# Kernel tuning notes

Measured on AMD Instinct MI355X. Metric: run time of the kernel, lower is better.

## Reference

```python
import jax, jax.numpy as jnp
import numpy as np

H, I, E, TOP_K = 2048, 1408, 16, 6
IS = 2816  # shared-expert intermediate = moe_intermediate_size * n_shared_experts
NORM_TOPK_PROB = False


def _silu_and_mul(gate_up):
    # gate_up: [..., 2*I] -> silu(gate) * up, [..., I]
    d = gate_up.shape[-1] // 2
    g, u = gate_up[..., :d], gate_up[..., d:]
    return jax.nn.silu(g) * u


def setup_inputs() -> dict:
    key = jax.random.key(0)
    ks = jax.random.split(key, 6)
    s = 0.02
    return {
        "x": jax.random.normal(ks[0], (1, 2048, H), jnp.float32),
        "gate_w": jax.random.normal(ks[1], (E, H), jnp.float32) * s,
        "w1": jax.random.normal(ks[2], (E, 2 * I, H), jnp.float32) * s,
        "w2": jax.random.normal(ks[3], (E, H, I), jnp.float32) * s,
        "shared_w1": jax.random.normal(ks[4], (2 * IS, H), jnp.float32) * s,
        "shared_w2": jax.random.normal(ks[5], (H, IS), jnp.float32) * s,
    }


def reference(x, gate_w, w1, w2, shared_w1, shared_w2):
    B, S, Hd = x.shape
    xf = x.reshape(-1, Hd)  # [T, H]
    T = xf.shape[0]

    # shared experts (dense MLP over all tokens)
    shared_out = _silu_and_mul(xf @ shared_w1.T) @ shared_w2.T  # [T, H]

    # router: softmax in fp32, then top-k
    logits = xf @ gate_w.T  # [T, E]
    probs = jax.nn.softmax(logits.astype(jnp.float32), axis=-1)
    routing_weights, selected = jax.lax.top_k(probs, TOP_K)  # [T, k]
    if NORM_TOPK_PROB:
        routing_weights = routing_weights / routing_weights.sum(-1, keepdims=True)

    # scatter top-k weights into dense [T, E] combine matrix (fused_moe equivalent)
    combine = jnp.zeros((T, E), jnp.float32).at[
        jnp.arange(T)[:, None], selected
    ].add(routing_weights).astype(x.dtype)

    # expert MLPs, combined with routing weights
    gate_up = jnp.einsum('th,eoh->teo', xf, w1)  # [T, E, 2I]
    act = _silu_and_mul(gate_up)                 # [T, E, I]
    moe_out = jnp.einsum('te,tei,ehi->th', combine, act, w2)  # [T, H]

    return (moe_out + shared_out).reshape(B, S, Hd)
```

## Files before the change

### kernel.cpp

```cpp
#include <hip/hip_runtime.h>
#include <hip/hip_bf16.h>
#include <cstdint>
#include <cstddef>


typedef __bf16 bf16;
typedef __bf16 bf16x8 __attribute__((ext_vector_type(8)));
typedef float  f32x4  __attribute__((ext_vector_type(4)));

constexpr int Hdim  = 2048;
constexpr int Idim  = 1408;
constexpr int NE    = 16;
constexpr int TOPK  = 6;
constexpr int ISdim = 2816;
constexpr int Ttok  = 2048;
constexpr int MAX_SLOTS = 14336;

__device__ __forceinline__ void gll16(const bf16* g, bf16* l) {
  __builtin_amdgcn_global_load_lds((__attribute__((address_space(1))) void*)(g),
                                   (__attribute__((address_space(3))) void*)(l),
                                   16, 0, 0);
}


__global__ void init_kernel(int* cnt, int* fill, int* tok_of_slot, float* wt_of_slot) {
  int i = blockIdx.x * 256 + threadIdx.x;
  if (i < NE) { cnt[i] = 0; fill[i] = 0; }
  if (i < MAX_SLOTS) { tok_of_slot[i] = -1; wt_of_slot[i] = 0.f; }
}

__global__ void cvt_x_kernel(const float* __restrict__ x, bf16* __restrict__ xb) {
  int i = (blockIdx.x * 256 + threadIdx.x) * 8;
  f32x4 f0 = *(const f32x4*)(x + i);
  f32x4 f1 = *(const f32x4*)(x + i + 4);
  bf16x8 v;
#pragma unroll
  for (int j = 0; j < 4; j++) { v[j] = (bf16)f0[j]; v[j + 4] = (bf16)f1[j]; }
  *(bf16x8*)(xb + i) = v;
}

__global__ void router_kernel(const float* __restrict__ x, const float* __restrict__ gw,
                              int* __restrict__ sel_e, float* __restrict__ sel_w,
                              int* __restrict__ cnt) {
  int t = blockIdx.x;
  int lane = threadIdx.x;
  const float* xr = x + (size_t)t * Hdim;
  float acc[NE];
#pragma unroll
  for (int e = 0; e < NE; e++) acc[e] = 0.f;
  for (int h = lane; h < Hdim; h += 64) {
    float xv = xr[h];
#pragma unroll
    for (int e = 0; e < NE; e++) acc[e] += xv * gw[e * Hdim + h];
  }
#pragma unroll
  for (int e = 0; e < NE; e++) {
#pragma unroll
    for (int off = 32; off > 0; off >>= 1) acc[e] += __shfl_xor(acc[e], off, 64);
  }
  if (lane == 0) {
    float m = acc[0];
#pragma unroll
    for (int e = 1; e < NE; e++) m = fmaxf(m, acc[e]);
    float p[NE]; float s = 0.f;
#pragma unroll
    for (int e = 0; e < NE; e++) { p[e] = __expf(acc[e] - m); s += p[e]; }
    float inv = 1.f / s;
    bool used[NE];
#pragma unroll
    for (int e = 0; e < NE; e++) used[e] = false;
    for (int k = 0; k < TOPK; k++) {
      int best = 0; float bv = -1.f;
      for (int e = 0; e < NE; e++) if (!used[e] && p[e] > bv) { bv = p[e]; best = e; }
      used[best] = true;
      sel_e[t * TOPK + k] = best;
      sel_w[t * TOPK + k] = bv * inv;
      atomicAdd(&cnt[best], 1);
    }
  }
}

__global__ void scan_kernel(const int* __restrict__ cnt, int* __restrict__ pbase,
                            int* __restrict__ mtiles) {
  if (threadIdx.x == 0 && blockIdx.x == 0) {
    int pb = 0;
    for (int e = 0; e < NE; e++) {
      pbase[e] = pb;
      int mt = (cnt[e] + 127) >> 7;
      mtiles[e] = mt;
      pb += mt * 128;
    }
  }
}

__global__ void assign_kernel(const int* __restrict__ sel_e, const float* __restrict__ sel_w,
                              const int* __restrict__ pbase, int* __restrict__ fill,
                              int* __restrict__ tok_of_slot, float* __restrict__ wt_of_slot) {
  int i = blockIdx.x * 256 + threadIdx.x;
  if (i >= Ttok * TOPK) return;
  int t = i / TOPK;
  int e = sel_e[i];
  int pos = atomicAdd(&fill[e], 1);
  int slot = pbase[e] + pos;
  tok_of_slot[slot] = t;
  wt_of_slot[slot] = sel_w[i];
}


template <bool GROUPED>
__global__ __launch_bounds__(256, 2)
void gateup_kernel(const bf16* __restrict__ Abase, const float* __restrict__ W,
                   bf16* __restrict__ Cact,
                   const int* __restrict__ tok_of_slot, const float* __restrict__ wt_of_slot,
                   const int* __restrict__ pbase, const int* __restrict__ mtiles,
                   int K, int Isz) {
  const int e = GROUPED ? blockIdx.z : 0;
  const int mt = blockIdx.y;
  if (GROUPED) { if (mt >= mtiles[e]) return; }
  const int row0 = (GROUPED ? pbase[e] : 0) + mt * 128;
  const int col0 = blockIdx.x * 64;
  const int tid = threadIdx.x;
  const int lane = tid & 63;
  const int wv = tid >> 6;
  const int wm = wv >> 1, wn = wv & 1;
  const int m16 = lane & 15, quad = lane >> 4;

  __shared__ __align__(16) bf16 ldsA[128 * 32];
  __shared__ __align__(16) bf16 ldsG[64 * 32];
  __shared__ __align__(16) bf16 ldsU[64 * 32];

  const int srow = tid >> 2;
  const int scol = (tid & 3) * 8;

  const bf16* aptr[2];
#pragma unroll
  for (int q = 0; q < 2; q++) {
    int r = row0 + q * 64 + srow;
    int tok = GROUPED ? tok_of_slot[r] : r;
    if (GROUPED && tok < 0) tok = 0;
    aptr[q] = Abase + (size_t)tok * K + scol;
  }
  const float* Wb = W + (size_t)e * 2 * Isz * K;
  const float* Grow = Wb + (size_t)(col0 + srow) * K + scol;
  const float* Urow = Wb + (size_t)(Isz + col0 + srow) * K + scol;

  f32x4 accg[4][2], accu[4][2];
#pragma unroll
  for (int i = 0; i < 4; i++)
#pragma unroll
    for (int j = 0; j < 2; j++)
#pragma unroll
      for (int r = 0; r < 4; r++) { accg[i][j][r] = 0.f; accu[i][j][r] = 0.f; }

  f32x4 gb0 = *(const f32x4*)(Grow);
  f32x4 gb1 = *(const f32x4*)(Grow + 4);
  f32x4 ub0 = *(const f32x4*)(Urow);
  f32x4 ub1 = *(const f32x4*)(Urow + 4);

  for (int k0 = 0; k0 < K; k0 += 32) {
    bf16x8 gv, uv;
#pragma unroll
    for (int j = 0; j < 4; j++) {
      gv[j] = (bf16)gb0[j]; gv[j + 4] = (bf16)gb1[j];
      uv[j] = (bf16)ub0[j]; uv[j + 4] = (bf16)ub1[j];
    }
    *(bf16x8*)(&ldsG[tid * 8]) = gv;
    *(bf16x8*)(&ldsU[tid * 8]) = uv;
#pragma unroll
    for (int q = 0; q < 2; q++) gll16(aptr[q] + k0, &ldsA[q * 2048 + tid * 8]);
    if (k0 + 32 < K) {
      gb0 = *(const f32x4*)(Grow + k0 + 32);
      gb1 = *(const f32x4*)(Grow + k0 + 36);
      ub0 = *(const f32x4*)(Urow + k0 + 32);
      ub1 = *(const f32x4*)(Urow + k0 + 36);
    }
    __syncthreads();
    bf16x8 af[4], gf[2], uf[2];
#pragma unroll
    for (int i = 0; i < 4; i++)
      af[i] = *(const bf16x8*)(&ldsA[(wm * 64 + i * 16 + m16) * 32 + quad * 8]);
#pragma unroll
    for (int j = 0; j < 2; j++) {
      gf[j] = *(const bf16x8*)(&ldsG[(wn * 32 + j * 16 + m16) * 32 + quad * 8]);
      uf[j] = *(const bf16x8*)(&ldsU[(wn * 32 + j * 16 + m16) * 32 + quad * 8]);
    }
#pragma unroll
    for (int i = 0; i < 4; i++)
#pragma unroll
      for (int j = 0; j < 2; j++) {
        accg[i][j] = __builtin_amdgcn_mfma_f32_16x16x32_bf16(af[i], gf[j], accg[i][j], 0, 0, 0);
        accu[i][j] = __builtin_amdgcn_mfma_f32_16x16x32_bf16(af[i], uf[j], accu[i][j], 0, 0, 0);
      }
    __syncthreads();
  }

#pragma unroll
  for (int i = 0; i < 4; i++) {
#pragma unroll
    for (int r = 0; r < 4; r++) {
      int grow = row0 + wm * 64 + i * 16 + quad * 4 + r;
      float scale = 1.f;
      if (GROUPED) scale = wt_of_slot[grow];
#pragma unroll
      for (int j = 0; j < 2; j++) {
        float g = accg[i][j][r];
        float u = accu[i][j][r];
        float a = g * u * scale / (1.f + __expf(-g));
        Cact[(size_t)grow * Isz + (col0 + wn * 32 + j * 16 + m16)] = (bf16)a;
      }
    }
  }
}


template <bool GROUPED>
__global__ __launch_bounds__(256, 2)
void down_kernel(const bf16* __restrict__ A, const float* __restrict__ W,
                 float* __restrict__ out, const int* __restrict__ tok_of_slot,
                 const int* __restrict__ pbase, const int* __restrict__ mtiles, int K) {
  const int e = GROUPED ? blockIdx.z : 0;
  const int mt = blockIdx.y;
  if (GROUPED) { if (mt >= mtiles[e]) return; }
  const int row0 = (GROUPED ? pbase[e] : 0) + mt * 128;
  const int col0 = blockIdx.x * 128;
  const int tid = threadIdx.x;
  const int lane = tid & 63;
  const int wv = tid >> 6;
  const int wm = wv >> 1, wn = wv & 1;
  const int m16 = lane & 15, quad = lane >> 4;

  __shared__ __align__(16) bf16 ldsA[128 * 32];
  __shared__ __align__(16) bf16 ldsB[128 * 32];

  const int srow = tid >> 2;
  const int scol = (tid & 3) * 8;

  const bf16* aptr[2];
#pragma unroll
  for (int q = 0; q < 2; q++)
    aptr[q] = A + (size_t)(row0 + q * 64 + srow) * K + scol;
  const float* Wb = W + (size_t)e * Hdim * K;
  const float* Brow[2];
#pragma unroll
  for (int q = 0; q < 2; q++)
    Brow[q] = Wb + (size_t)(col0 + q * 64 + srow) * K + scol;

  f32x4 acc[4][4];
#pragma unroll
  for (int i = 0; i < 4; i++)
#pragma unroll
    for (int j = 0; j < 4; j++)
#pragma unroll
      for (int r = 0; r < 4; r++) acc[i][j][r] = 0.f;

  f32x4 bb[2][2];
#pragma unroll
  for (int q = 0; q < 2; q++) {
    bb[q][0] = *(const f32x4*)(Brow[q]);
    bb[q][1] = *(const f32x4*)(Brow[q] + 4);
  }

  for (int k0 = 0; k0 < K; k0 += 32) {
#pragma unroll
    for (int q = 0; q < 2; q++) {
      bf16x8 bv;
#pragma unroll
      for (int j = 0; j < 4; j++) { bv[j] = (bf16)bb[q][0][j]; bv[j + 4] = (bf16)bb[q][1][j]; }
      *(bf16x8*)(&ldsB[q * 2048 + tid * 8]) = bv;
      gll16(aptr[q] + k0, &ldsA[q * 2048 + tid * 8]);
    }
    if (k0 + 32 < K) {
#pragma unroll
      for (int q = 0; q < 2; q++) {
        bb[q][0] = *(const f32x4*)(Brow[q] + k0 + 32);
        bb[q][1] = *(const f32x4*)(Brow[q] + k0 + 36);
      }
    }
    __syncthreads();
    bf16x8 af[4], bfr[4];
#pragma unroll
    for (int i = 0; i < 4; i++)
      af[i] = *(const bf16x8*)(&ldsA[(wm * 64 + i * 16 + m16) * 32 + quad * 8]);
#pragma unroll
    for (int j = 0; j < 4; j++)
      bfr[j] = *(const bf16x8*)(&ldsB[(wn * 64 + j * 16 + m16) * 32 + quad * 8]);
#pragma unroll
    for (int i = 0; i < 4; i++)
#pragma unroll
      for (int j = 0; j < 4; j++)
        acc[i][j] = __builtin_amdgcn_mfma_f32_16x16x32_bf16(af[i], bfr[j], acc[i][j], 0, 0, 0);
    __syncthreads();
  }

#pragma unroll
  for (int i = 0; i < 4; i++) {
#pragma unroll
    for (int r = 0; r < 4; r++) {
      int grow = row0 + wm * 64 + i * 16 + quad * 4 + r;
      int tok;
      if (GROUPED) {
        tok = tok_of_slot[grow];
        if (tok < 0) continue;
      } else {
        tok = grow;
      }
      float* orow = out + (size_t)tok * Hdim;
#pragma unroll
      for (int j = 0; j < 4; j++) {
        int col = col0 + wn * 64 + j * 16 + m16;
        if (GROUPED) atomicAdd(orow + col, acc[i][j][r]);
        else orow[col] = acc[i][j][r];
      }
    }
  }
}


extern "C" void kernel_launch(void* const* d_in, const int* in_sizes, int n_in,
                              void* d_out, int out_size, void* d_ws, size_t ws_size,
                              hipStream_t stream) {
  (void)in_sizes; (void)n_in; (void)out_size; (void)ws_size;
  const float* x   = (const float*)d_in[0];
  const float* gw  = (const float*)d_in[1];
  const float* w1  = (const float*)d_in[2];
  const float* w2  = (const float*)d_in[3];
  const float* sw1 = (const float*)d_in[4];
  const float* sw2 = (const float*)d_in[5];
  float* out = (float*)d_out;

  char* ws = (char*)d_ws;
  size_t off = 0;
  auto alloc = [&](size_t bytes) -> void* {
    void* p = ws + off;
    off += (bytes + 255) & ~(size_t)255;
    return p;
  };
  int*   cnt   = (int*)alloc(NE * 4);
  int*   fill  = (int*)alloc(NE * 4);
  int*   pbase = (int*)alloc(NE * 4);
  int*   mtl   = (int*)alloc(NE * 4);
  int*   sel_e = (int*)alloc((size_t)Ttok * TOPK * 4);
  float* sel_w = (float*)alloc((size_t)Ttok * TOPK * 4);
  int*   tok   = (int*)alloc((size_t)MAX_SLOTS * 4);
  float* wt    = (float*)alloc((size_t)MAX_SLOTS * 4);
  bf16*  xb    = (bf16*)alloc((size_t)Ttok * Hdim * 2);
  bf16*  actx  = (bf16*)alloc((size_t)MAX_SLOTS * Idim * 2);
  bf16*  acts  = (bf16*)alloc((size_t)Ttok * ISdim * 2);

  init_kernel<<<(MAX_SLOTS + 255) / 256, 256, 0, stream>>>(cnt, fill, tok, wt);
  cvt_x_kernel<<<(Ttok * Hdim / 8 + 255) / 256, 256, 0, stream>>>(x, xb);
  router_kernel<<<Ttok, 64, 0, stream>>>(x, gw, sel_e, sel_w, cnt);
  scan_kernel<<<1, 64, 0, stream>>>(cnt, pbase, mtl);
  assign_kernel<<<(Ttok * TOPK + 255) / 256, 256, 0, stream>>>(sel_e, sel_w, pbase, fill, tok, wt);

  gateup_kernel<true><<<dim3(Idim / 64, 16, NE), 256, 0, stream>>>(
      xb, w1, actx, tok, wt, pbase, mtl, Hdim, Idim);
  gateup_kernel<false><<<dim3(ISdim / 64, Ttok / 128, 1), 256, 0, stream>>>(
      xb, sw1, acts, nullptr, nullptr, nullptr, nullptr, Hdim, ISdim);
  down_kernel<false><<<dim3(Hdim / 128, Ttok / 128, 1), 256, 0, stream>>>(
      acts, sw2, out, nullptr, nullptr, nullptr, ISdim);
  down_kernel<true><<<dim3(Hdim / 128, 16, NE), 256, 0, stream>>>(
      actx, w2, out, tok, pbase, mtl, Idim);
}
```

Before: 1.448 ms.

## Pre-convert weights to bf16 and widen grouped GEMM M-tiles to 256 rows

When the workspace is large enough, all four weight tensors are converted to bf16 by separate kernels, and the GEMMs then load B tiles with direct global-to-LDS copies instead of loading fp32 and converting in registers. The warp layout changes so each wave owns a slab of rows and all columns, and the grouped expert GEMMs use 256-row M tiles, which raises weight reuse per tile at the cost of more padding slots. The extra conversion passes read every fp32 weight once and write a bf16 copy on every call, adding memory traffic. Register pressure also rises with the larger per-wave accumulator arrays.

```diff
diff --git a/kernel.cpp b/kernel.cpp
--- a/kernel.cpp
+++ b/kernel.cpp
@@ -14,9 +14,10 @@
 constexpr int TOPK  = 6;
 constexpr int ISdim = 2816;
 constexpr int Ttok  = 2048;
-constexpr int MAX_SLOTS = 14336;
-
-__device__ __forceinline__ void gll16(const bf16* g, bf16* l) {
+constexpr int BMG   = 256;
+constexpr int MAX_SLOTS = 16384;
+
+__device__ __forceinline__ void gll16(const void* g, void* l) {
   __builtin_amdgcn_global_load_lds((__attribute__((address_space(1))) void*)(g),
                                    (__attribute__((address_space(3))) void*)(l),
                                    16, 0, 0);
@@ -29,14 +30,15 @@
   if (i < MAX_SLOTS) { tok_of_slot[i] = -1; wt_of_slot[i] = 0.f; }
 }
 
-__global__ void cvt_x_kernel(const float* __restrict__ x, bf16* __restrict__ xb) {
-  int i = (blockIdx.x * 256 + threadIdx.x) * 8;
-  f32x4 f0 = *(const f32x4*)(x + i);
-  f32x4 f1 = *(const f32x4*)(x + i + 4);
+__global__ void cvt_kernel(const float* __restrict__ src, bf16* __restrict__ dst, int n8) {
+  int i = blockIdx.x * 256 + threadIdx.x;
+  if (i >= n8) return;
+  f32x4 f0 = *(const f32x4*)(src + (size_t)i * 8);
+  f32x4 f1 = *(const f32x4*)(src + (size_t)i * 8 + 4);
   bf16x8 v;
 #pragma unroll
   for (int j = 0; j < 4; j++) { v[j] = (bf16)f0[j]; v[j + 4] = (bf16)f1[j]; }
-  *(bf16x8*)(xb + i) = v;
+  *(bf16x8*)(dst + (size_t)i * 8) = v;
 }
 
 __global__ void router_kernel(const float* __restrict__ x, const float* __restrict__ gw,
@@ -86,9 +88,9 @@
     int pb = 0;
     for (int e = 0; e < NE; e++) {
       pbase[e] = pb;
-      int mt = (cnt[e] + 127) >> 7;
+      int mt = (cnt[e] + BMG - 1) / BMG;
       mtiles[e] = mt;
-      pb += mt * 128;
+      pb += mt * BMG;
     }
   }
 }
@@ -107,87 +109,103 @@
 }
 
 
-template <bool GROUPED>
+template <bool GROUPED, bool BF16B, int BM>
 __global__ __launch_bounds__(256, 2)
-void gateup_kernel(const bf16* __restrict__ Abase, const float* __restrict__ W,
+void gateup_kernel(const bf16* __restrict__ Abase, const void* __restrict__ Wv,
                    bf16* __restrict__ Cact,
                    const int* __restrict__ tok_of_slot, const float* __restrict__ wt_of_slot,
                    const int* __restrict__ pbase, const int* __restrict__ mtiles,
                    int K, int Isz) {
+  constexpr int NQ = BM / 64;
+  constexpr int WROWS = BM / 4;
+  constexpr int NI = WROWS / 16;
   const int e = GROUPED ? blockIdx.z : 0;
   const int mt = blockIdx.y;
   if (GROUPED) { if (mt >= mtiles[e]) return; }
-  const int row0 = (GROUPED ? pbase[e] : 0) + mt * 128;
+  const int row0 = (GROUPED ? pbase[e] : 0) + mt * BM;
   const int col0 = blockIdx.x * 64;
   const int tid = threadIdx.x;
   const int lane = tid & 63;
   const int wv = tid >> 6;
-  const int wm = wv >> 1, wn = wv & 1;
   const int m16 = lane & 15, quad = lane >> 4;
 
-  __shared__ __align__(16) bf16 ldsA[128 * 32];
+  __shared__ __align__(16) bf16 ldsA[BM * 32];
   __shared__ __align__(16) bf16 ldsG[64 * 32];
   __shared__ __align__(16) bf16 ldsU[64 * 32];
 
   const int srow = tid >> 2;
   const int scol = (tid & 3) * 8;
 
-  const bf16* aptr[2];
-#pragma unroll
-  for (int q = 0; q < 2; q++) {
+  const bf16* aptr[NQ];
+#pragma unroll
+  for (int q = 0; q < NQ; q++) {
     int r = row0 + q * 64 + srow;
     int tok = GROUPED ? tok_of_slot[r] : r;
     if (GROUPED && tok < 0) tok = 0;
     aptr[q] = Abase + (size_t)tok * K + scol;
   }
-  const float* Wb = W + (size_t)e * 2 * Isz * K;
-  const float* Grow = Wb + (size_t)(col0 + srow) * K + scol;
-  const float* Urow = Wb + (size_t)(Isz + col0 + srow) * K + scol;
-
-  f32x4 accg[4][2], accu[4][2];
-#pragma unroll
-  for (int i = 0; i < 4; i++)
-#pragma unroll
-    for (int j = 0; j < 2; j++)
+
+  const bf16* gptrB = nullptr; const bf16* uptrB = nullptr;
+  const float* GrowF = nullptr; const float* UrowF = nullptr;
+  f32x4 gb0, gb1, ub0, ub1;
+  if constexpr (BF16B) {
+    const bf16* Wb = (const bf16*)Wv + (size_t)e * 2 * Isz * K;
+    gptrB = Wb + (size_t)(col0 + srow) * K + scol;
+    uptrB = Wb + (size_t)(Isz + col0 + srow) * K + scol;
+  } else {
+    const float* Wb = (const float*)Wv + (size_t)e * 2 * Isz * K;
+    GrowF = Wb + (size_t)(col0 + srow) * K + scol;
+    UrowF = Wb + (size_t)(Isz + col0 + srow) * K + scol;
+    gb0 = *(const f32x4*)(GrowF);
+    gb1 = *(const f32x4*)(GrowF + 4);
+    ub0 = *(const f32x4*)(UrowF);
+    ub1 = *(const f32x4*)(UrowF + 4);
+  }
+
+  f32x4 accg[NI][4], accu[NI][4];
+#pragma unroll
+  for (int i = 0; i < NI; i++)
+#pragma unroll
+    for (int j = 0; j < 4; j++)
 #pragma unroll
       for (int r = 0; r < 4; r++) { accg[i][j][r] = 0.f; accu[i][j][r] = 0.f; }
 
-  f32x4 gb0 = *(const f32x4*)(Grow);
-  f32x4 gb1 = *(const f32x4*)(Grow + 4);
-  f32x4 ub0 = *(const f32x4*)(Urow);
-  f32x4 ub1 = *(const f32x4*)(Urow + 4);
-
   for (int k0 = 0; k0 < K; k0 += 32) {
-    bf16x8 gv, uv;
+    if constexpr (BF16B) {
+      gll16(gptrB + k0, &ldsG[tid * 8]);
+      gll16(uptrB + k0, &ldsU[tid * 8]);
+    } else {
+      bf16x8 gv, uv;
+#pragma unroll
+      for (int j = 0; j < 4; j++) {
+        gv[j] = (bf16)gb0[j]; gv[j + 4] = (bf16)gb1[j];
+        uv[j] = (bf16)ub0[j]; uv[j + 4] = (bf16)ub1[j];
+      }
+      *(bf16x8*)(&ldsG[tid * 8]) = gv;
+      *(bf16x8*)(&ldsU[tid * 8]) = uv;
+      if (k0 + 32 < K) {
+        gb0 = *(const f32x4*)(GrowF + k0 + 32);
+        gb1 = *(const f32x4*)(GrowF + k0 + 36);
+        ub0 = *(const f32x4*)(UrowF + k0 + 32);
+        ub1 = *(const f32x4*)(UrowF + k0 + 36);
+      }
+    }
+#pragma unroll
+    for (int q = 0; q < NQ; q++) gll16(aptr[q] + k0, &ldsA[q * 2048 + tid * 8]);
+    __syncthreads();
+    bf16x8 af[NI], gf[4], uf[4];
+#pragma unroll
+    for (int i = 0; i < NI; i++)
+      af[i] = *(const bf16x8*)(&ldsA[(wv * WROWS + i * 16 + m16) * 32 + quad * 8]);
 #pragma unroll
     for (int j = 0; j < 4; j++) {
-      gv[j] = (bf16)gb0[j]; gv[j + 4] = (bf16)gb1[j];
-      uv[j] = (bf16)ub0[j]; uv[j + 4] = (bf16)ub1[j];
-    }
-    *(bf16x8*)(&ldsG[tid * 8]) = gv;
-    *(bf16x8*)(&ldsU[tid * 8]) = uv;
-#pragma unroll
-    for (int q = 0; q < 2; q++) gll16(aptr[q] + k0, &ldsA[q * 2048 + tid * 8]);
-    if (k0 + 32 < K) {
-      gb0 = *(const f32x4*)(Grow + k0 + 32);
-      gb1 = *(const f32x4*)(Grow + k0 + 36);
-      ub0 = *(const f32x4*)(Urow + k0 + 32);
-      ub1 = *(const f32x4*)(Urow + k0 + 36);
-    }
-    __syncthreads();
-    bf16x8 af[4], gf[2], uf[2];
-#pragma unroll
-    for (int i = 0; i < 4; i++)
-      af[i] = *(const bf16x8*)(&ldsA[(wm * 64 + i * 16 + m16) * 32 + quad * 8]);
-#pragma unroll
-    for (int j = 0; j < 2; j++) {
-      gf[j] = *(const bf16x8*)(&ldsG[(wn * 32 + j * 16 + m16) * 32 + quad * 8]);
-      uf[j] = *(const bf16x8*)(&ldsU[(wn * 32 + j * 16 + m16) * 32 + quad * 8]);
-    }
-#pragma unroll
-    for (int i = 0; i < 4; i++)
-#pragma unroll
-      for (int j = 0; j < 2; j++) {
+      gf[j] = *(const bf16x8*)(&ldsG[(j * 16 + m16) * 32 + quad * 8]);
+      uf[j] = *(const bf16x8*)(&ldsU[(j * 16 + m16) * 32 + quad * 8]);
+    }
+#pragma unroll
+    for (int i = 0; i < NI; i++)
+#pragma unroll
+      for (int j = 0; j < 4; j++) {
         accg[i][j] = __builtin_amdgcn_mfma_f32_16x16x32_bf16(af[i], gf[j], accg[i][j], 0, 0, 0);
         accu[i][j] = __builtin_amdgcn_mfma_f32_16x16x32_bf16(af[i], uf[j], accu[i][j], 0, 0, 0);
       }
@@ -195,108 +213,122 @@
   }
 
 #pragma unroll
-  for (int i = 0; i < 4; i++) {
+  for (int i = 0; i < NI; i++) {
 #pragma unroll
     for (int r = 0; r < 4; r++) {
-      int grow = row0 + wm * 64 + i * 16 + quad * 4 + r;
+      int grow = row0 + wv * WROWS + i * 16 + quad * 4 + r;
       float scale = 1.f;
       if (GROUPED) scale = wt_of_slot[grow];
 #pragma unroll
-      for (int j = 0; j < 2; j++) {
+      for (int j = 0; j < 4; j++) {
         float g = accg[i][j][r];
         float u = accu[i][j][r];
         float a = g * u * scale / (1.f + __expf(-g));
-        Cact[(size_t)grow * Isz + (col0 + wn * 32 + j * 16 + m16)] = (bf16)a;
-      }
-    }
-  }
-}
-
-
-template <bool GROUPED>
+        Cact[(size_t)grow * Isz + (col0 + j * 16 + m16)] = (bf16)a;
+      }
+    }
+  }
+}
+
+
+template <bool GROUPED, bool BF16B, int BM>
 __global__ __launch_bounds__(256, 2)
-void down_kernel(const bf16* __restrict__ A, const float* __restrict__ W,
+void down_kernel(const bf16* __restrict__ A, const void* __restrict__ Wv,
                  float* __restrict__ out, const int* __restrict__ tok_of_slot,
                  const int* __restrict__ pbase, const int* __restrict__ mtiles, int K) {
+  constexpr int NQ = BM / 64;
+  constexpr int WROWS = BM / 4;
+  constexpr int NI = WROWS / 16;
   const int e = GROUPED ? blockIdx.z : 0;
   const int mt = blockIdx.y;
   if (GROUPED) { if (mt >= mtiles[e]) return; }
-  const int row0 = (GROUPED ? pbase[e] : 0) + mt * 128;
+  const int row0 = (GROUPED ? pbase[e] : 0) + mt * BM;
   const int col0 = blockIdx.x * 128;
   const int tid = threadIdx.x;
   const int lane = tid & 63;
   const int wv = tid >> 6;
-  const int wm = wv >> 1, wn = wv & 1;
   const int m16 = lane & 15, quad = lane >> 4;
 
-  __shared__ __align__(16) bf16 ldsA[128 * 32];
+  __shared__ __align__(16) bf16 ldsA[BM * 32];
   __shared__ __align__(16) bf16 ldsB[128 * 32];
 
   const int srow = tid >> 2;
   const int scol = (tid & 3) * 8;
 
-  const bf16* aptr[2];
-#pragma unroll
-  for (int q = 0; q < 2; q++)
+  const bf16* aptr[NQ];
+#pragma unroll
+  for (int q = 0; q < NQ; q++)
     aptr[q] = A + (size_t)(row0 + q * 64 + srow) * K + scol;
-  const float* Wb = W + (size_t)e * Hdim * K;
-  const float* Brow[2];
-#pragma unroll
-  for (int q = 0; q < 2; q++)
-    Brow[q] = Wb + (size_t)(col0 + q * 64 + srow) * K + scol;
-
-  f32x4 acc[4][4];
-#pragma unroll
-  for (int i = 0; i < 4; i++)
-#pragma unroll
-    for (int j = 0; j < 4; j++)
+
+  const bf16* bptrB[2] = {nullptr, nullptr};
+  const float* BrowF[2] = {nullptr, nullptr};
+  f32x4 bb[2][2];
+  if constexpr (BF16B) {
+    const bf16* Wb = (const bf16*)Wv + (size_t)e * Hdim * K;
+#pragma unroll
+    for (int q = 0; q < 2; q++)
+      bptrB[q] = Wb + (size_t)(col0 + q * 64 + srow) * K + scol;
+  } else {
+    const float* Wb = (const float*)Wv + (size_t)e * Hdim * K;
+#pragma unroll
+    for (int q = 0; q < 2; q++) {
+      BrowF[q] = Wb + (size_t)(col0 + q * 64 + srow) * K + scol;
+      bb[q][0] = *(const f32x4*)(BrowF[q]);
+      bb[q][1] = *(const f32x4*)(BrowF[q] + 4);
+    }
+  }
+
+  f32x4 acc[NI][8];
+#pragma unroll
+  for (int i = 0; i < NI; i++)
+#pragma unroll
+    for (int j = 0; j < 8; j++)
 #pragma unroll
       for (int r = 0; r < 4; r++) acc[i][j][r] = 0.f;
 
-  f32x4 bb[2][2];
-#pragma unroll
-  for (int q = 0; q < 2; q++) {
-    bb[q][0] = *(const f32x4*)(Brow[q]);
-    bb[q][1] = *(const f32x4*)(Brow[q] + 4);
-  }
-
   for (int k0 = 0; k0 < K; k0 += 32) {
-#pragma unroll
-    for (int q = 0; q < 2; q++) {
-      bf16x8 bv;
-#pragma unroll
-      for (int j = 0; j < 4; j++) { bv[j] = (bf16)bb[q][0][j]; bv[j + 4] = (bf16)bb[q][1][j]; }
-      *(bf16x8*)(&ldsB[q * 2048 + tid * 8]) = bv;
-      gll16(aptr[q] + k0, &ldsA[q * 2048 + tid * 8]);
-    }
-    if (k0 + 32 < K) {
+    if constexpr (BF16B) {
+#pragma unroll
+      for (int q = 0; q < 2; q++) gll16(bptrB[q] + k0, &ldsB[q * 2048 + tid * 8]);
+    } else {
 #pragma unroll
       for (int q = 0; q < 2; q++) {
-        bb[q][0] = *(const f32x4*)(Brow[q] + k0 + 32);
-        bb[q][1] = *(const f32x4*)(Brow[q] + k0 + 36);
-      }
-    }
+        bf16x8 bv;
+#pragma unroll
+        for (int j = 0; j < 4; j++) { bv[j] = (bf16)bb[q][0][j]; bv[j + 4] = (bf16)bb[q][1][j]; }
+        *(bf16x8*)(&ldsB[q * 2048 + tid * 8]) = bv;
+      }
+      if (k0 + 32 < K) {
+#pragma unroll
+        for (int q = 0; q < 2; q++) {
+          bb[q][0] = *(const f32x4*)(BrowF[q] + k0 + 32);
+          bb[q][1] = *(const f32x4*)(BrowF[q] + k0 + 36);
+        }
+      }
+    }
+#pragma unroll
+    for (int q = 0; q < NQ; q++) gll16(aptr[q] + k0, &ldsA[q * 2048 + tid * 8]);
     __syncthreads();
-    bf16x8 af[4], bfr[4];
-#pragma unroll
-    for (int i = 0; i < 4; i++)
-      af[i] = *(const bf16x8*)(&ldsA[(wm * 64 + i * 16 + m16) * 32 + quad * 8]);
-#pragma unroll
-    for (int j = 0; j < 4; j++)
-      bfr[j] = *(const bf16x8*)(&ldsB[(wn * 64 + j * 16 + m16) * 32 + quad * 8]);
-#pragma unroll
-    for (int i = 0; i < 4; i++)
-#pragma unroll
-      for (int j = 0; j < 4; j++)
+    bf16x8 af[NI], bfr[8];
+#pragma unroll
+    for (int i = 0; i < NI; i++)
+      af[i] = *(const bf16x8*)(&ldsA[(wv * WROWS + i * 16 + m16) * 32 + quad * 8]);
+#pragma unroll
+    for (int j = 0; j < 8; j++)
+      bfr[j] = *(const bf16x8*)(&ldsB[(j * 16 + m16) * 32 + quad * 8]);
+#pragma unroll
+    for (int i = 0; i < NI; i++)
+#pragma unroll
+      for (int j = 0; j < 8; j++)
         acc[i][j] = __builtin_amdgcn_mfma_f32_16x16x32_bf16(af[i], bfr[j], acc[i][j], 0, 0, 0);
     __syncthreads();
   }
 
 #pragma unroll
-  for (int i = 0; i < 4; i++) {
+  for (int i = 0; i < NI; i++) {
 #pragma unroll
     for (int r = 0; r < 4; r++) {
-      int grow = row0 + wm * 64 + i * 16 + quad * 4 + r;
+      int grow = row0 + wv * WROWS + i * 16 + quad * 4 + r;
       int tok;
       if (GROUPED) {
         tok = tok_of_slot[grow];
@@ -306,8 +338,8 @@
       }
       float* orow = out + (size_t)tok * Hdim;
 #pragma unroll
-      for (int j = 0; j < 4; j++) {
-        int col = col0 + wn * 64 + j * 16 + m16;
+      for (int j = 0; j < 8; j++) {
+        int col = col0 + j * 16 + m16;
         if (GROUPED) atomicAdd(orow + col, acc[i][j][r]);
         else orow[col] = acc[i][j][r];
       }
@@ -319,7 +351,7 @@
 extern "C" void kernel_launch(void* const* d_in, const int* in_sizes, int n_in,
                               void* d_out, int out_size, void* d_ws, size_t ws_size,
                               hipStream_t stream) {
-  (void)in_sizes; (void)n_in; (void)out_size; (void)ws_size;
+  (void)in_sizes; (void)n_in; (void)out_size;
   const float* x   = (const float*)d_in[0];
   const float* gw  = (const float*)d_in[1];
   const float* w1  = (const float*)d_in[2];
@@ -347,18 +379,46 @@
   bf16*  actx  = (bf16*)alloc((size_t)MAX_SLOTS * Idim * 2);
   bf16*  acts  = (bf16*)alloc((size_t)Ttok * ISdim * 2);
 
+  const size_t n_w1  = (size_t)NE * 2 * Idim * Hdim;
+  const size_t n_w2  = (size_t)NE * Hdim * Idim;
+  const size_t n_sw1 = (size_t)2 * ISdim * Hdim;
+  const size_t n_sw2 = (size_t)Hdim * ISdim;
+  size_t off_base = off;
+  bf16* w1b  = (bf16*)alloc(n_w1 * 2);
+  bf16* w2b  = (bf16*)alloc(n_w2 * 2);
+  bf16* sw1b = (bf16*)alloc(n_sw1 * 2);
+  bf16* sw2b = (bf16*)alloc(n_sw2 * 2);
+  const bool use_bf16w = (off <= ws_size);
+  (void)off_base;
+
   init_kernel<<<(MAX_SLOTS + 255) / 256, 256, 0, stream>>>(cnt, fill, tok, wt);
-  cvt_x_kernel<<<(Ttok * Hdim / 8 + 255) / 256, 256, 0, stream>>>(x, xb);
+  cvt_kernel<<<((int)(Ttok * (size_t)Hdim / 8) + 255) / 256, 256, 0, stream>>>(x, xb, Ttok * Hdim / 8);
   router_kernel<<<Ttok, 64, 0, stream>>>(x, gw, sel_e, sel_w, cnt);
   scan_kernel<<<1, 64, 0, stream>>>(cnt, pbase, mtl);
   assign_kernel<<<(Ttok * TOPK + 255) / 256, 256, 0, stream>>>(sel_e, sel_w, pbase, fill, tok, wt);
 
-  gateup_kernel<true><<<dim3(Idim / 64, 16, NE), 256, 0, stream>>>(
-      xb, w1, actx, tok, wt, pbase, mtl, Hdim, Idim);
-  gateup_kernel<false><<<dim3(ISdim / 64, Ttok / 128, 1), 256, 0, stream>>>(
-      xb, sw1, acts, nullptr, nullptr, nullptr, nullptr, Hdim, ISdim);
-  down_kernel<false><<<dim3(Hdim / 128, Ttok / 128, 1), 256, 0, stream>>>(
-      acts, sw2, out, nullptr, nullptr, nullptr, ISdim);
-  down_kernel<true><<<dim3(Hdim / 128, 16, NE), 256, 0, stream>>>(
-      actx, w2, out, tok, pbase, mtl, Idim);
-}
+  if (use_bf16w) {
+    cvt_kernel<<<((int)(n_w1 / 8) + 255) / 256, 256, 0, stream>>>(w1, w1b, (int)(n_w1 / 8));
+    cvt_kernel<<<((int)(n_w2 / 8) + 255) / 256, 256, 0, stream>>>(w2, w2b, (int)(n_w2 / 8));
+    cvt_kernel<<<((int)(n_sw1 / 8) + 255) / 256, 256, 0, stream>>>(sw1, sw1b, (int)(n_sw1 / 8));
+    cvt_kernel<<<((int)(n_sw2 / 8) + 255) / 256, 256, 0, stream>>>(sw2, sw2b, (int)(n_sw2 / 8));
+
+    gateup_kernel<true, true, BMG><<<dim3(Idim / 64, Ttok / BMG, NE), 256, 0, stream>>>(
+        xb, w1b, actx, tok, wt, pbase, mtl, Hdim, Idim);
+    gateup_kernel<false, true, 128><<<dim3(ISdim / 64, Ttok / 128, 1), 256, 0, stream>>>(
+        xb, sw1b, acts, nullptr, nullptr, nullptr, nullptr, Hdim, ISdim);
+    down_kernel<false, true, 128><<<dim3(Hdim / 128, Ttok / 128, 1), 256, 0, stream>>>(
+        acts, sw2b, out, nullptr, nullptr, nullptr, ISdim);
+    down_kernel<true, true, BMG><<<dim3(Hdim / 128, Ttok / BMG, NE), 256, 0, stream>>>(
+        actx, w2b, out, tok, pbase, mtl, Idim);
+  } else {
+    gateup_kernel<true, false, BMG><<<dim3(Idim / 64, Ttok / BMG, NE), 256, 0, stream>>>(
+        xb, w1, actx, tok, wt, pbase, mtl, Hdim, Idim);
+    gateup_kernel<false, false, 128><<<dim3(ISdim / 64, Ttok / 128, 1), 256, 0, stream>>>(
+        xb, sw1, acts, nullptr, nullptr, nullptr, nullptr, Hdim, ISdim);
+    down_kernel<false, false, 128><<<dim3(Hdim / 128, Ttok / 128, 1), 256, 0, stream>>>(
+        acts, sw2, out, nullptr, nullptr, nullptr, ISdim);
+    down_kernel<true, false, BMG><<<dim3(Hdim / 128, Ttok / BMG, NE), 256, 0, stream>>>(
+        actx, w2, out, tok, pbase, mtl, Idim);
+  }
+}
```

Result: faster. 1.414 ms (-2.4%).
